# Kernel optimization log

Measured on AMD Instinct MI355X. Metric: run time of the kernel, lower is better.

Reference implementation:

```python
import jax, jax.numpy as jnp
import numpy as np

N = 500_000
EPS_IN = 1e-6   # point-in-box tolerance (matches mmcv diff_iou_rotated)
EPS_IOU = 1e-8


def _box2corners(box):
    # box [N,7]: (x,y,z,w,l,h,alpha) -> BEV rectangle corners [N,4,2]
    x, y = box[:, 0], box[:, 1]
    w, l, a = box[:, 3], box[:, 4], box[:, 6]
    tx = jnp.array([0.5, -0.5, -0.5, 0.5], dtype=box.dtype)
    ty = jnp.array([0.5, 0.5, -0.5, -0.5], dtype=box.dtype)
    x4 = tx[None, :] * w[:, None]
    y4 = ty[None, :] * l[:, None]
    c, s = jnp.cos(a)[:, None], jnp.sin(a)[:, None]
    cx = x4 * c - y4 * s + x[:, None]
    cy = x4 * s + y4 * c + y[:, None]
    return jnp.stack([cx, cy], axis=-1)


def _cross2(a, b):
    return a[..., 0] * b[..., 1] - a[..., 1] * b[..., 0]


def _edge_intersections(c1, c2):
    # all 4x4 edge-pair segment intersections -> pts [N,16,2], mask [N,16]
    p1 = c1[:, :, None, :]                         # [N,4,1,2]
    p2 = jnp.roll(c1, -1, axis=1)[:, :, None, :]
    q1 = c2[:, None, :, :]                         # [N,1,4,2]
    q2 = jnp.roll(c2, -1, axis=1)[:, None, :, :]
    r = p2 - p1
    s = q2 - q1
    den = _cross2(r, s)
    den_safe = jnp.where(den == 0, 1.0, den)
    t = _cross2(q1 - p1, s) / den_safe
    u = _cross2(q1 - p1, r) / den_safe
    mask = (den != 0) & (t > 0) & (t < 1) & (u > 0) & (u < 1)
    pts = jnp.where(mask[..., None], p1 + t[..., None] * r, 0.0)
    n = c1.shape[0]
    return pts.reshape(n, 16, 2), mask.reshape(n, 16)


def _points_in_box(pts, corners):
    # pts [N,4,2] inside rotated rect given by corners [N,4,2]
    a = corners[:, 0:1]
    b = corners[:, 1:2]
    d = corners[:, 3:4]
    ab, ad, ap = b - a, d - a, pts - a
    pab = jnp.sum(ap * ab, -1) / jnp.sum(ab * ab, -1)
    pad_ = jnp.sum(ap * ad, -1) / jnp.sum(ad * ad, -1)
    return (pab > -EPS_IN) & (pab < 1 + EPS_IN) & (pad_ > -EPS_IN) & (pad_ < 1 + EPS_IN)


def _polygon_area(verts, mask):
    # verts [N,24,2], mask [N,24]: sort valid vertices CCW around their mean,
    # close the polygon, shoelace area. Invalid slots set to first valid vertex
    # so they contribute zero cross terms.
    maskf = mask.astype(verts.dtype)
    nv = jnp.maximum(jnp.sum(maskf, axis=1, keepdims=True), 1.0)
    mean = jnp.sum(verts * maskf[..., None], axis=1, keepdims=True) / nv[..., None]
    cen = verts - mean
    ang = jnp.where(mask, jnp.arctan2(cen[..., 1], cen[..., 0]), 1e9)
    order = jnp.argsort(ang, axis=1)
    s = jnp.take_along_axis(cen, order[..., None], axis=1)
    m = jnp.take_along_axis(mask, order, axis=1)
    v0 = s[:, 0:1, :]  # first valid vertex (valid slots sort first)
    s = jnp.where(m[..., None], s, v0)
    s_next = jnp.roll(s, -1, axis=1)
    return 0.5 * jnp.abs(jnp.sum(_cross2(s, s_next), axis=1))


def _rotated_iou_3d(pred, target):
    c1 = _box2corners(pred)
    c2 = _box2corners(target)
    inter_pts, inter_mask = _edge_intersections(c1, c2)
    in12 = _points_in_box(c1, c2)
    in21 = _points_in_box(c2, c1)
    verts = jnp.concatenate([c1, c2, inter_pts], axis=1)      # [N,24,2]
    mask = jnp.concatenate([in12, in21, inter_mask], axis=1)  # [N,24]
    inter_area = _polygon_area(verts, mask)
    zt = jnp.minimum(pred[:, 2] + 0.5 * pred[:, 5], target[:, 2] + 0.5 * target[:, 5])
    zb = jnp.maximum(pred[:, 2] - 0.5 * pred[:, 5], target[:, 2] - 0.5 * target[:, 5])
    inter_vol = inter_area * jnp.clip(zt - zb, 0.0)
    v1 = pred[:, 3] * pred[:, 4] * pred[:, 5]
    v2 = target[:, 3] * target[:, 4] * target[:, 5]
    return inter_vol / (v1 + v2 - inter_vol + EPS_IOU)


def setup_inputs() -> dict:
    key = jax.random.key(0)
    k1, k2, k3, k4 = jax.random.split(key, 4)
    centers = jax.random.uniform(k1, (N, 3), jnp.float32, -50.0, 50.0)
    dims = jax.random.uniform(k2, (N, 3), jnp.float32, 1.0, 4.0)
    alpha = jax.random.uniform(k3, (N, 1), jnp.float32, -np.pi, np.pi)
    target = jnp.concatenate([centers, dims, alpha], axis=1)
    noise_scale = jnp.array([0.5, 0.5, 0.3, 0.2, 0.2, 0.2, 0.1], jnp.float32)
    pred = target + jax.random.normal(k4, (N, 7), jnp.float32) * noise_scale
    pred = pred.at[:, 3:6].set(jnp.maximum(pred[:, 3:6], 0.1))  # keep dims positive
    return {"pred": pred, "target": target}


def reference(pred, target):
    # RotatedIoU3DLoss(mode='iou', reduction='mean', loss_weight=1.0)
    return 1.0 * jnp.mean(1.0 - _rotated_iou_3d(pred, target))
```

## Files before the change

### kernel.cpp

```cpp
#include <hip/hip_runtime.h>
#include <math.h>

#define EPS_IOU 1e-8f
#define IPB 512
#define NF (IPB * 7)

__device__ __forceinline__ float clip_sum(const float px[4], const float py[4],
                                          const float qx[4], const float qy[4])
{
    float ex[4], ey[4];
#pragma unroll
    for (int j = 0; j < 4; ++j) {
        ex[j] = qx[(j + 1) & 3] - qx[j];
        ey[j] = qy[(j + 1) & 3] - qy[j];
    }
    float D[4][4];
#pragma unroll
    for (int i = 0; i < 4; ++i) {
#pragma unroll
        for (int j = 0; j < 4; ++j) {
            D[i][j] = ex[j] * (py[i] - qy[j]) - ey[j] * (px[i] - qx[j]);
        }
    }
    float s = 0.0f;
#pragma unroll
    for (int i = 0; i < 4; ++i) {
        const int i1 = (i + 1) & 3;
        float t0 = 0.0f, t1 = 1.0f;
#pragma unroll
        for (int j = 0; j < 4; ++j) {
            float d0 = D[i][j], d1 = D[i1][j];
            float den = d0 - d1;
            float r = d0 * __builtin_amdgcn_rcpf(den);
            t1 = (den > 0.0f) ? fminf(t1, r) : t1;
            t0 = (den < 0.0f) ? fmaxf(t0, r) : t0;
            t0 = (den == 0.0f && d0 < 0.0f) ? 2.0f : t0;
        }
        float dx = px[i1] - px[i], dy = py[i1] - py[i];
        float x0 = px[i] + t0 * dx, y0 = py[i] + t0 * dy;
        float x1 = px[i] + t1 * dx, y1 = py[i] + t1 * dy;
        float cr = x0 * y1 - y0 * x1;
        s += (t0 < t1) ? cr : 0.0f;
    }
    return s;
}

__device__ __forceinline__ float one_loss(const float* __restrict__ P,
                                          const float* __restrict__ T)
{
    float px = P[0], py = P[1], pz = P[2], pw = P[3], pl = P[4], ph = P[5], pa = P[6];
    float qx = T[0], qy = T[1], qz = T[2], qw = T[3], ql = T[4], qh = T[5], qa = T[6];

    const float TXc[4] = {0.5f, -0.5f, -0.5f, 0.5f};
    const float TYc[4] = {0.5f, 0.5f, -0.5f, -0.5f};
    float ax[4], ay[4], bx[4], by[4];
    float ca, sa, cb, sb;
    __sincosf(pa, &sa, &ca);
    __sincosf(qa, &sb, &cb);
#pragma unroll
    for (int k = 0; k < 4; ++k) {
        float xx = TXc[k] * pw, yy = TYc[k] * pl;
        ax[k] = xx * ca - yy * sa + px;
        ay[k] = xx * sa + yy * ca + py;
        float x2 = TXc[k] * qw, y2 = TYc[k] * ql;
        bx[k] = x2 * cb - y2 * sb + qx;
        by[k] = x2 * sb + y2 * cb + qy;
    }

    float s2 = clip_sum(ax, ay, bx, by) + clip_sum(bx, by, ax, ay);
    float inter_area = 0.5f * fabsf(s2);

    float zt = fminf(pz + 0.5f * ph, qz + 0.5f * qh);
    float zb = fmaxf(pz - 0.5f * ph, qz - 0.5f * qh);
    float hz = fmaxf(zt - zb, 0.0f);
    float inter_vol = inter_area * hz;
    float v1 = pw * pl * ph;
    float v2 = qw * ql * qh;
    float iou = inter_vol * __builtin_amdgcn_rcpf(v1 + v2 - inter_vol + EPS_IOU);
    return 1.0f - iou;
}

__global__ __launch_bounds__(256) void iou_main_kernel(
    const float* __restrict__ pred,
    const float* __restrict__ target,
    float* __restrict__ partial,
    int n, float invN)
{
    __shared__ float sP[NF];
    __shared__ float sT[NF];

    const int base = blockIdx.x * IPB;
    const int rem = min(IPB, n - base);
    const int nf = rem * 7;

    const float4* gp = (const float4*)(pred + (size_t)base * 7);
    const float4* gt = (const float4*)(target + (size_t)base * 7);
    float4* lp = (float4*)sP;
    float4* lt = (float4*)sT;
    for (int k = threadIdx.x; k * 4 < nf; k += 256) {
        if (k * 4 + 3 < nf) {
            lp[k] = gp[k];
            lt[k] = gt[k];
        } else {
            for (int c = k * 4; c < nf; ++c) {
                sP[c] = pred[(size_t)base * 7 + c];
                sT[c] = target[(size_t)base * 7 + c];
            }
        }
    }
    __syncthreads();

    float loss = 0.0f;
#pragma unroll
    for (int it = 0; it < 2; ++it) {
        int j = threadIdx.x + it * 256;
        if (j < rem) loss += one_loss(sP + 7 * j, sT + 7 * j) * invN;
    }

#pragma unroll
    for (int off = 32; off > 0; off >>= 1)
        loss += __shfl_down(loss, off, 64);
    __shared__ float wsum[4];
    int lane = threadIdx.x & 63;
    int wid = threadIdx.x >> 6;
    if (lane == 0) wsum[wid] = loss;
    __syncthreads();
    if (threadIdx.x == 0)
        partial[blockIdx.x] = wsum[0] + wsum[1] + wsum[2] + wsum[3];
}

__global__ __launch_bounds__(256) void iou_reduce_kernel(
    const float* __restrict__ partial, float* __restrict__ out, int g)
{
    float s = 0.0f;
    for (int k = threadIdx.x; k < g; k += 256) s += partial[k];
#pragma unroll
    for (int off = 32; off > 0; off >>= 1)
        s += __shfl_down(s, off, 64);
    __shared__ float wsum[4];
    int lane = threadIdx.x & 63;
    int wid = threadIdx.x >> 6;
    if (lane == 0) wsum[wid] = s;
    __syncthreads();
    if (threadIdx.x == 0)
        out[0] = wsum[0] + wsum[1] + wsum[2] + wsum[3];
}

extern "C" void kernel_launch(void* const* d_in, const int* in_sizes, int n_in,
                              void* d_out, int out_size, void* d_ws, size_t ws_size,
                              hipStream_t stream) {
    const float* pred = (const float*)d_in[0];
    const float* target = (const float*)d_in[1];
    float* out = (float*)d_out;
    float* partial = (float*)d_ws;
    int n = in_sizes[0] / 7;

    int grid = (n + IPB - 1) / IPB;
    iou_main_kernel<<<grid, 256, 0, stream>>>(pred, target, partial, n,
                                              1.0f / (float)n);
    iou_reduce_kernel<<<1, 256, 0, stream>>>(partial, out, grid);
}
```

Baseline: 85.06 us.

## Replace polygon edge clipping with slab-based clipping in box-local frame

Rewrites the 2D intersection area computation by moving one box into the other's local axis-aligned frame and clipping each edge with a ray/slab test against the axis-aligned half-extents. The area comes from shoelace terms written in closed form using edge parameters, which removes the 4x4 half-plane distance matrix and per-edge reciprocal loops. It cuts the ALU work per pair. The risk is numerical: edges exactly parallel to the axes give infinite reciprocals, and NaNs can appear from 0*inf in the slab test.

```diff
diff --git a/kernel.cpp b/kernel.cpp
--- a/kernel.cpp
+++ b/kernel.cpp
@@ -5,44 +5,15 @@
 #define IPB 512
 #define NF (IPB * 7)
 
-__device__ __forceinline__ float clip_sum(const float px[4], const float py[4],
-                                          const float qx[4], const float qy[4])
+__device__ __forceinline__ float slab_dt(float sx, float sy,
+                                         float rdx, float rdy,
+                                         float hx, float hy)
 {
-    float ex[4], ey[4];
-#pragma unroll
-    for (int j = 0; j < 4; ++j) {
-        ex[j] = qx[(j + 1) & 3] - qx[j];
-        ey[j] = qy[(j + 1) & 3] - qy[j];
-    }
-    float D[4][4];
-#pragma unroll
-    for (int i = 0; i < 4; ++i) {
-#pragma unroll
-        for (int j = 0; j < 4; ++j) {
-            D[i][j] = ex[j] * (py[i] - qy[j]) - ey[j] * (px[i] - qx[j]);
-        }
-    }
-    float s = 0.0f;
-#pragma unroll
-    for (int i = 0; i < 4; ++i) {
-        const int i1 = (i + 1) & 3;
-        float t0 = 0.0f, t1 = 1.0f;
-#pragma unroll
-        for (int j = 0; j < 4; ++j) {
-            float d0 = D[i][j], d1 = D[i1][j];
-            float den = d0 - d1;
-            float r = d0 * __builtin_amdgcn_rcpf(den);
-            t1 = (den > 0.0f) ? fminf(t1, r) : t1;
-            t0 = (den < 0.0f) ? fmaxf(t0, r) : t0;
-            t0 = (den == 0.0f && d0 < 0.0f) ? 2.0f : t0;
-        }
-        float dx = px[i1] - px[i], dy = py[i1] - py[i];
-        float x0 = px[i] + t0 * dx, y0 = py[i] + t0 * dy;
-        float x1 = px[i] + t1 * dx, y1 = py[i] + t1 * dy;
-        float cr = x0 * y1 - y0 * x1;
-        s += (t0 < t1) ? cr : 0.0f;
-    }
-    return s;
+    float tx1 = (-hx - sx) * rdx, tx2 = (hx - sx) * rdx;
+    float ty1 = (-hy - sy) * rdy, ty2 = (hy - sy) * rdy;
+    float t0 = fmaxf(fmaxf(fminf(tx1, tx2), fminf(ty1, ty2)), 0.0f);
+    float t1 = fminf(fminf(fmaxf(tx1, tx2), fmaxf(ty1, ty2)), 1.0f);
+    return fmaxf(t1 - t0, 0.0f);
 }
 
 __device__ __forceinline__ float one_loss(const float* __restrict__ P,
@@ -51,24 +22,60 @@
     float px = P[0], py = P[1], pz = P[2], pw = P[3], pl = P[4], ph = P[5], pa = P[6];
     float qx = T[0], qy = T[1], qz = T[2], qw = T[3], ql = T[4], qh = T[5], qa = T[6];
 
-    const float TXc[4] = {0.5f, -0.5f, -0.5f, 0.5f};
-    const float TYc[4] = {0.5f, 0.5f, -0.5f, -0.5f};
-    float ax[4], ay[4], bx[4], by[4];
+    float hpx = 0.5f * pw, hpy = 0.5f * pl;
+    float hqx = 0.5f * qw, hqy = 0.5f * ql;
+
     float ca, sa, cb, sb;
     __sincosf(pa, &sa, &ca);
     __sincosf(qa, &sb, &cb);
-#pragma unroll
-    for (int k = 0; k < 4; ++k) {
-        float xx = TXc[k] * pw, yy = TYc[k] * pl;
-        ax[k] = xx * ca - yy * sa + px;
-        ay[k] = xx * sa + yy * ca + py;
-        float x2 = TXc[k] * qw, y2 = TYc[k] * ql;
-        bx[k] = x2 * cb - y2 * sb + qx;
-        by[k] = x2 * sb + y2 * cb + qy;
-    }
+    float ct = ca * cb + sa * sb;
+    float st = sb * ca - sa * cb;
 
-    float s2 = clip_sum(ax, ay, bx, by) + clip_sum(bx, by, ax, ay);
-    float inter_area = 0.5f * fabsf(s2);
+    float dxw = qx - px, dyw = qy - py;
+    float cx_ =  ca * dxw + sa * dyw;
+    float cy_ = -sa * dxw + ca * dyw;
+
+    float ux = ct * hqx, uy = st * hqx;
+    float vx = -st * hqy, vy = ct * hqy;
+
+    float r2ux = __builtin_amdgcn_rcpf(2.0f * ux);
+    float r2uy = __builtin_amdgcn_rcpf(2.0f * uy);
+    float r2vx = __builtin_amdgcn_rcpf(2.0f * vx);
+    float r2vy = __builtin_amdgcn_rcpf(2.0f * vy);
+
+    float upx = ux + vx, upy = uy + vy;
+    float umx = ux - vx, umy = uy - vy;
+    float dq0 = slab_dt(cx_ + upx, cy_ + upy, -r2ux, -r2uy, hpx, hpy);
+    float dq1 = slab_dt(cx_ - umx, cy_ - umy, -r2vx, -r2vy, hpx, hpy);
+    float dq2 = slab_dt(cx_ - upx, cy_ - upy,  r2ux,  r2uy, hpx, hpy);
+    float dq3 = slab_dt(cx_ + umx, cy_ + umy,  r2vx,  r2vy, hpx, hpy);
+
+    float Cu = cx_ * uy - cy_ * ux;
+    float Cv = cx_ * vy - cy_ * vx;
+    float W2 = 2.0f * (hqx * hqy);
+    float Cu2 = 2.0f * Cu, Cv2 = 2.0f * Cv;
+    float area2 = dq0 * (W2 - Cu2) + dq1 * (W2 - Cv2)
+                + dq2 * (W2 + Cu2) + dq3 * (W2 + Cv2);
+
+    float u2x = ct * hpx, u2y = -st * hpx;
+    float v2x = st * hpy, v2y = ct * hpy;
+    float c2x = -(ct * cx_ + st * cy_);
+    float c2y = st * cx_ - ct * cy_;
+
+    float r2u2x = __builtin_amdgcn_rcpf(2.0f * u2x);
+    float r2u2y = __builtin_amdgcn_rcpf(2.0f * u2y);
+    float r2v2x = __builtin_amdgcn_rcpf(2.0f * v2x);
+    float r2v2y = __builtin_amdgcn_rcpf(2.0f * v2y);
+
+    float up2x = u2x + v2x, up2y = u2y + v2y;
+    float um2x = u2x - v2x, um2y = u2y - v2y;
+    float dtp = slab_dt(c2x + up2x, c2y + up2y, -r2u2x, -r2u2y, hqx, hqy)
+              + slab_dt(c2x - um2x, c2y - um2y, -r2v2x, -r2v2y, hqx, hqy)
+              + slab_dt(c2x - up2x, c2y - up2y,  r2u2x,  r2u2y, hqx, hqy)
+              + slab_dt(c2x + um2x, c2y + um2y,  r2v2x,  r2v2y, hqx, hqy);
+    area2 += dtp * (2.0f * (hpx * hpy));
+
+    float inter_area = 0.5f * fabsf(area2);
 
     float zt = fminf(pz + 0.5f * ph, qz + 0.5f * qh);
     float zb = fmaxf(pz - 0.5f * ph, qz - 0.5f * qh);
```

Measured after the change: 76.46 us. 1.11x faster.
